# Kernel optimization log

Measured on AMD Instinct MI355X. Metric: run time of the kernel, lower is better.

## Reference

```python
import jax, jax.numpy as jnp
import numpy as np


def conv_transpose_4s2p1(x, w, b):
    # torch ConvTranspose2d(k=4, s=2, p=1). w is torch layout [Cin, Cout, 4, 4].
    # Equivalent to a regular conv with lhs_dilation=2, per-side pad k-1-p=2,
    # spatially-flipped kernel and in/out channels swapped.
    wk = jnp.flip(w, (2, 3)).transpose(1, 0, 2, 3)  # [Cout, Cin, 4, 4]
    y = jax.lax.conv_general_dilated(
        x, wk, window_strides=(1, 1), padding=((2, 2), (2, 2)),
        lhs_dilation=(2, 2), dimension_numbers=('NCHW', 'OIHW', 'NCHW'))
    return y + b[None, :, None, None]


def pac_conv_transpose_3s1p1(y, guide, w, b):
    # PacConvTranspose2d(k=3, s=1, p=1): with stride 1 this equals pacconv2d on
    # input zero-padded by k-1-p = 1, with the weight in/out-permuted and flipped
    # (pacnet native impl). Adaptive kernel: K_kk = exp(-0.5*||g_nbr - g_center||^2)
    # computed on the (zero-padded) guide at output resolution.
    B, C, H, W = y.shape
    wk = jnp.flip(w, (2, 3)).transpose(1, 0, 2, 3)  # [Cout, Cin, 3, 3]
    Co = wk.shape[0]
    gp = jnp.pad(guide, ((0, 0), (0, 0), (1, 1), (1, 1)))
    yp = jnp.pad(y, ((0, 0), (0, 0), (1, 1), (1, 1)))
    out = jnp.zeros((B, Co, H, W), y.dtype)
    for i in range(3):  # fixed 3x3 taps, not a data-dim loop
        for j in range(3):
            gn = gp[:, :, i:i + H, j:j + W]                # [B,Cg,H,W] neighbor
            d = gn - guide
            k = jnp.exp(-0.5 * jnp.sum(d * d, axis=1))      # [B,H,W] gaussian kernel
            yn = yp[:, :, i:i + H, j:j + W]                # [B,C,H,W]
            out = out + jnp.einsum('oc,bchw->bohw', wk[:, :, i, j], yn * k[:, None])
    return out + b[None, :, None, None]


def setup_inputs() -> dict:
    key = jax.random.key(0)
    k1, k2, k3, k4, k5, k6 = jax.random.split(key, 6)
    B, Cin, Cout, H, W = 4, 256, 128, 64, 64
    x = jax.random.normal(k1, (B, Cin, H, W), jnp.float32)
    # guide scaled so ||diff||^2 over 128 channels stays O(1-10) and the
    # gaussian kernel is not numerically degenerate
    guide = 0.08 * jax.random.normal(k2, (B, Cout, 2 * H, 2 * W), jnp.float32)
    w1 = jax.random.normal(k3, (Cin, Cout, 4, 4), jnp.float32) / np.sqrt(Cin * 16)
    b1 = 0.01 * jax.random.normal(k4, (Cout,), jnp.float32)
    w2 = jax.random.normal(k5, (Cout, Cout, 3, 3), jnp.float32) / np.sqrt(Cout * 9)
    b2 = 0.01 * jax.random.normal(k6, (Cout,), jnp.float32)
    return {'x': x, 'guide': guide, 'w1': w1, 'b1': b1, 'w2': w2, 'b2': b2}


def reference(x, guide, w1, b1, w2, b2):
    y = conv_transpose_4s2p1(x, w1, b1)          # [B, Cout, 2H, 2W]
    out = pac_conv_transpose_3s1p1(y, guide, w2, b2)
    return out
```

## Files before the change

### kernel.cpp

```cpp
#include <hip/hip_runtime.h>

#define B_  4
#define C1  256
#define C2  128
#define HH  64
#define WW  64
#define H2  128
#define W2  128

using short8  = __attribute__((ext_vector_type(8))) short;
using floatx4 = __attribute__((ext_vector_type(4))) float;
typedef unsigned short ushort_t;

#define W1C_OFF 0u
#define W1C_ELEMS (4 * 4 * 128 * 256)
#define W2C_OFF (W1C_ELEMS * 2u)
#define W2C_ELEMS (9 * 128 * 128)
#define KG_OFF  (W2C_OFF + W2C_ELEMS * 2u)
#define KG_ELEMS (B_ * H2 * 9 * W2)
#define XT_OFF  (KG_OFF + KG_ELEMS * 4u)
#define XT_ELEMS (B_ * HH * WW * C1)
#define Y_OFF   (XT_OFF + XT_ELEMS * 2u)
#define Y_ELEMS (B_ * H2 * W2 * C2)

static __device__ __forceinline__ ushort_t f2bf(float f) {
    union { float f; unsigned u; } v; v.f = f;
    unsigned r = v.u + 0x7FFFu + ((v.u >> 16) & 1u);
    return (ushort_t)(r >> 16);
}

__global__ void w1c_kernel(const float* __restrict__ w1, ushort_t* __restrict__ w1c) {
    int i = blockIdx.x * 256 + threadIdx.x;
    const int ci  = i & 255;
    const int co  = (i >> 8) & 127;
    const int tap = (i >> 15) & 3;
    const int cls = i >> 17;
    const int kh  = (cls >> 1) + 2 * (tap >> 1);
    const int kw  = (cls & 1) + 2 * (tap & 1);
    w1c[i] = f2bf(w1[((ci * C2 + co) * 4 + kh) * 4 + kw]);
}

__global__ void w2c_kernel(const float* __restrict__ w2, ushort_t* __restrict__ w2c) {
    int i = blockIdx.x * 256 + threadIdx.x;
    const int ci  = i & 127;
    const int o   = (i >> 7) & 127;
    const int tap = i >> 14;
    const int fi  = 2 - tap / 3;
    const int fj  = 2 - tap % 3;
    w2c[i] = f2bf(w2[((ci * C2 + o) * 3 + fi) * 3 + fj]);
}

__global__ __launch_bounds__(256) void xt_kernel(const float* __restrict__ x,
                                                 ushort_t* __restrict__ xT) {
    const int ih = blockIdx.x;
    const int b  = blockIdx.y;
    const int tid = threadIdx.x;
    __shared__ ushort_t tile[64 * 72];

    for (int chunk = 0; chunk < 4; ++chunk) {
        const int ci0 = chunk * 64;
        if (chunk) __syncthreads();
#pragma unroll
        for (int it = 0; it < 16; ++it) {
            const int cc = it * 4 + (tid >> 6);
            const int iw = tid & 63;
            const float v = x[(((size_t)b * C1 + ci0 + cc) * HH + ih) * WW + iw];
            tile[iw * 72 + cc] = f2bf(v);
        }
        __syncthreads();
#pragma unroll
        for (int it = 0; it < 2; ++it) {
            const int i  = it * 256 + tid;
            const int iw = i >> 3;
            const int t  = i & 7;
            const int4 v = *reinterpret_cast<const int4*>(&tile[iw * 72 + t * 8]);
            *reinterpret_cast<int4*>(&xT[(((size_t)(b * HH + ih) * WW) + iw) * C1 + ci0 + t * 8]) = v;
        }
    }
}

__global__ __launch_bounds__(512) void k_kernel(const float* __restrict__ guide,
                                                float* __restrict__ kg) {
    const int h = blockIdx.x;
    const int b = blockIdx.y;
    const int tid = threadIdx.x;
    const int cq  = tid >> 7;
    const int n   = tid & 127;

    float acc[9];
#pragma unroll
    for (int t = 0; t < 9; ++t) acc[t] = 0.f;

    const float* gb = guide + (size_t)b * C2 * H2 * W2;
    for (int c = cq * 32; c < cq * 32 + 32; ++c) {
        const float* grow = gb + (c * H2 + h) * W2;
        const float gc = grow[n];
#pragma unroll
        for (int di = 0; di < 3; ++di) {
            const int hh = h + di - 1;
            const bool rv = (hh >= 0) && (hh < H2);
            const float* gr = gb + (c * H2 + (rv ? hh : 0)) * W2;
#pragma unroll
            for (int dj = 0; dj < 3; ++dj) {
                const int col = n + dj - 1;
                const bool cv = rv && (col >= 0) && (col < W2);
                const float gn = cv ? gr[col] : 0.f;
                const float d = gn - gc;
                acc[di * 3 + dj] += d * d;
            }
        }
    }

    __shared__ float part[4][9][128];
#pragma unroll
    for (int t = 0; t < 9; ++t) part[cq][t][n] = acc[t];
    __syncthreads();

    for (int i = tid; i < 1152; i += 512) {
        const int t  = i >> 7;
        const int nn = i & 127;
        const float s = part[0][t][nn] + part[1][t][nn] + part[2][t][nn] + part[3][t][nn];
        kg[(size_t)(b * H2 + h) * 1152 + i] = __expf(-0.5f * s);
    }
}

__global__ __launch_bounds__(256, 2) void deconv_mfma(const ushort_t* __restrict__ xT,
                                                      const ushort_t* __restrict__ w1c,
                                                      const float* __restrict__ b1,
                                                      ushort_t* __restrict__ y) {
    const int pwc = blockIdx.x;
    const int pr  = blockIdx.y;
    const int b   = blockIdx.z;
    const int base_oh = (pr >> 1) * 4 + (pr & 1);
    const int p    = (base_oh + 1) & 1;
    const int ihA0 = (base_oh + 1 - p) >> 1;
    const int pwp  = 1 - pwc;
    const int cls  = p * 2 + pwp;

    const int tid  = threadIdx.x;
    const int lane = tid & 63;
    const int wave = tid >> 6;
    const int wm   = (wave & 1) * 64;
    const int wn   = (wave >> 1) * 64;
    const int quad = lane >> 4;
    const int l15  = lane & 15;

    __shared__ __align__(16) ushort_t lds[2 * 128 * 72];
    ushort_t* As = lds;
    ushort_t* Bs = lds + 128 * 72;

    floatx4 acc[4][4];
#pragma unroll
    for (int mi = 0; mi < 4; ++mi)
#pragma unroll
        for (int ni = 0; ni < 4; ++ni) acc[mi][ni] = (floatx4)0.f;

    for (int kc = 0; kc < 4; ++kc) {
        const int ci0 = kc * 64;
        for (int tap = 0; tap < 4; ++tap) {
            const int th = tap >> 1, tw = tap & 1;
            __syncthreads();
#pragma unroll
            for (int it = 0; it < 4; ++it) {
                const int i   = it * 256 + tid;
                const int row = i >> 3;
                const int t   = i & 7;
                const int4 v = *reinterpret_cast<const int4*>(
                    &w1c[((size_t)(cls * 4 + tap) * 128 + row) * 256 + ci0 + t * 8]);
                *reinterpret_cast<int4*>(&As[row * 72 + t * 8]) = v;
            }
#pragma unroll
            for (int it = 0; it < 4; ++it) {
                const int i   = it * 256 + tid;
                const int row = i >> 3;
                const int t   = i & 7;
                const int rh  = row >> 6;
                const int n64 = row & 63;
                const int ih  = ihA0 + rh - th;
                const int iw  = n64 + pwc - tw;
                int4 v = make_int4(0, 0, 0, 0);
                if (ih >= 0 && ih < HH && iw >= 0 && iw < WW)
                    v = *reinterpret_cast<const int4*>(
                        &xT[(((size_t)(b * HH + ih) * WW) + iw) * C1 + ci0 + t * 8]);
                *reinterpret_cast<int4*>(&Bs[row * 72 + t * 8]) = v;
            }
            __syncthreads();
#pragma unroll
            for (int k2 = 0; k2 < 2; ++k2) {
                short8 af[4], bfr[4];
#pragma unroll
                for (int mi = 0; mi < 4; ++mi)
                    af[mi] = *reinterpret_cast<const short8*>(
                        &As[(wm + mi * 16 + l15) * 72 + k2 * 32 + quad * 8]);
#pragma unroll
                for (int ni = 0; ni < 4; ++ni)
                    bfr[ni] = *reinterpret_cast<const short8*>(
                        &Bs[(wn + ni * 16 + l15) * 72 + k2 * 32 + quad * 8]);
#pragma unroll
                for (int mi = 0; mi < 4; ++mi)
#pragma unroll
                    for (int ni = 0; ni < 4; ++ni)
                        acc[mi][ni] = __builtin_amdgcn_mfma_f32_16x16x32_bf16(
                            af[mi], bfr[ni], acc[mi][ni], 0, 0, 0);
            }
        }
    }

    __syncthreads();
    ushort_t* Ot = lds;
#pragma unroll
    for (int mi = 0; mi < 4; ++mi)
#pragma unroll
        for (int ni = 0; ni < 4; ++ni) {
            const int n = wn + ni * 16 + l15;
#pragma unroll
            for (int r = 0; r < 4; ++r) {
                const int co = wm + mi * 16 + quad * 4 + r;
                Ot[n * 136 + co] = f2bf(acc[mi][ni][r] + b1[co]);
            }
        }
    __syncthreads();
#pragma unroll
    for (int it = 0; it < 8; ++it) {
        const int i   = it * 256 + tid;
        const int n   = i >> 4;
        const int t   = i & 15;
        const int rh  = n >> 6;
        const int n64 = n & 63;
        const int oh  = base_oh + 2 * rh;
        const int ow  = 2 * n64 + pwc;
        const int4 v = *reinterpret_cast<const int4*>(&Ot[n * 136 + t * 8]);
        *reinterpret_cast<int4*>(&y[(((size_t)(b * H2 + oh) * W2) + ow) * C2 + t * 8]) = v;
    }
}

__global__ __launch_bounds__(256, 2) void pac_mfma(const ushort_t* __restrict__ y,
                                                   const float* __restrict__ kg,
                                                   const ushort_t* __restrict__ w2c,
                                                   const float* __restrict__ b2,
                                                   float* __restrict__ out) {
    const int h = blockIdx.x;
    const int b = blockIdx.y;

    const int tid  = threadIdx.x;
    const int lane = tid & 63;
    const int wave = tid >> 6;
    const int wm   = (wave & 1) * 64;
    const int wn   = (wave >> 1) * 64;
    const int quad = lane >> 4;
    const int l15  = lane & 15;

    __shared__ __align__(16) ushort_t As[128 * 136];
    __shared__ __align__(16) ushort_t Ys[130 * 136];
    __shared__ float k_lds[9 * 128];

    for (int i = tid; i < 1152; i += 256)
        k_lds[i] = kg[(size_t)(b * H2 + h) * 1152 + i];

    float out_acc[4][4][4];
#pragma unroll
    for (int mi = 0; mi < 4; ++mi)
#pragma unroll
        for (int ni = 0; ni < 4; ++ni)
#pragma unroll
            for (int r = 0; r < 4; ++r) out_acc[mi][ni][r] = 0.f;

    for (int di = 0; di < 3; ++di) {
        const int hh = h + di - 1;
        if (hh < 0 || hh >= H2) continue;
        __syncthreads();
#pragma unroll
        for (int it = 0; it < 8; ++it) {
            const int i  = it * 256 + tid;
            const int r  = i >> 4;
            const int t  = i & 15;
            const int4 v = *reinterpret_cast<const int4*>(
                &y[(((size_t)(b * H2 + hh) * W2) + r) * C2 + t * 8]);
            *reinterpret_cast<int4*>(&Ys[(r + 1) * 136 + t * 8]) = v;
        }
        if (tid < 32) {
            const int ra = (tid < 16) ? 0 : 129;
            const int t  = tid & 15;
            *reinterpret_cast<int4*>(&Ys[ra * 136 + t * 8]) = make_int4(0, 0, 0, 0);
        }

        for (int dj = 0; dj < 3; ++dj) {
            const int tap = di * 3 + dj;
            __syncthreads();
#pragma unroll
            for (int it = 0; it < 8; ++it) {
                const int i   = it * 256 + tid;
                const int row = i >> 4;
                const int t   = i & 15;
                const int4 v = *reinterpret_cast<const int4*>(
                    &w2c[((size_t)tap * 128 + row) * 128 + t * 8]);
                *reinterpret_cast<int4*>(&As[row * 136 + t * 8]) = v;
            }
            __syncthreads();

            floatx4 acc[4][4];
#pragma unroll
            for (int mi = 0; mi < 4; ++mi)
#pragma unroll
                for (int ni = 0; ni < 4; ++ni) acc[mi][ni] = (floatx4)0.f;

#pragma unroll
            for (int kc = 0; kc < 4; ++kc) {
                short8 af[4], bfr[4];
#pragma unroll
                for (int mi = 0; mi < 4; ++mi)
                    af[mi] = *reinterpret_cast<const short8*>(
                        &As[(wm + mi * 16 + l15) * 136 + kc * 32 + quad * 8]);
#pragma unroll
                for (int ni = 0; ni < 4; ++ni)
                    bfr[ni] = *reinterpret_cast<const short8*>(
                        &Ys[(wn + ni * 16 + l15 + dj) * 136 + kc * 32 + quad * 8]);
#pragma unroll
                for (int mi = 0; mi < 4; ++mi)
#pragma unroll
                    for (int ni = 0; ni < 4; ++ni)
                        acc[mi][ni] = __builtin_amdgcn_mfma_f32_16x16x32_bf16(
                            af[mi], bfr[ni], acc[mi][ni], 0, 0, 0);
            }
            float kv[4];
#pragma unroll
            for (int ni = 0; ni < 4; ++ni)
                kv[ni] = k_lds[tap * 128 + wn + ni * 16 + l15];
#pragma unroll
            for (int mi = 0; mi < 4; ++mi)
#pragma unroll
                for (int ni = 0; ni < 4; ++ni)
#pragma unroll
                    for (int r = 0; r < 4; ++r)
                        out_acc[mi][ni][r] += kv[ni] * acc[mi][ni][r];
        }
    }

#pragma unroll
    for (int mi = 0; mi < 4; ++mi)
#pragma unroll
        for (int ni = 0; ni < 4; ++ni) {
            const int w = wn + ni * 16 + l15;
#pragma unroll
            for (int r = 0; r < 4; ++r) {
                const int o = wm + mi * 16 + quad * 4 + r;
                out[(((size_t)b * C2 + o) * H2 + h) * W2 + w] = out_acc[mi][ni][r] + b2[o];
            }
        }
}

extern "C" void kernel_launch(void* const* d_in, const int* in_sizes, int n_in,
                              void* d_out, int out_size, void* d_ws, size_t ws_size,
                              hipStream_t stream) {
    const float* x     = (const float*)d_in[0];
    const float* guide = (const float*)d_in[1];
    const float* w1    = (const float*)d_in[2];
    const float* b1    = (const float*)d_in[3];
    const float* w2    = (const float*)d_in[4];
    const float* b2    = (const float*)d_in[5];
    float* out = (float*)d_out;

    ushort_t* w1c = (ushort_t*)((char*)d_ws + W1C_OFF);
    ushort_t* w2c = (ushort_t*)((char*)d_ws + W2C_OFF);
    float*    kg  = (float*)((char*)d_ws + KG_OFF);
    ushort_t* xT  = (ushort_t*)((char*)d_ws + XT_OFF);
    ushort_t* y   = (ushort_t*)((char*)d_ws + Y_OFF);

    w1c_kernel<<<W1C_ELEMS / 256, 256, 0, stream>>>(w1, w1c);
    w2c_kernel<<<W2C_ELEMS / 256, 256, 0, stream>>>(w2, w2c);
    xt_kernel<<<dim3(HH, B_), 256, 0, stream>>>(x, xT);
    k_kernel<<<dim3(H2, B_), 512, 0, stream>>>(guide, kg);
    deconv_mfma<<<dim3(2, 64, B_), 256, 0, stream>>>(xT, w1c, b1, y);
    pac_mfma<<<dim3(H2, B_), 256, 0, stream>>>(y, kg, w2c, b2, out);
}
```

Measured before the change: 209.8 us.

## Read GEMM weight fragments directly from global memory and stage full-K activations

Both MFMA kernels now load the A (weight) fragments straight from global/L2 memory instead of staging them through LDS. The deconv kernel stages all 256 input channels of B per tap in one LDS buffer, and the PAC kernel drops its per-tap weight LDS copy, which removes most barriers. The weight-conversion kernels are rewritten for coalesced vector reads, and the transpose kernel now converts to bf16 after the LDS transpose. The trade is fewer syncs and less LDS traffic against higher global/L2 load latency on the MFMA operand path, which can now stall the matrix instructions.

New measurement: 227.7 us. 1.09x slower.

```diff
diff --git a/kernel.cpp b/kernel.cpp
--- a/kernel.cpp
+++ b/kernel.cpp
@@ -29,25 +29,39 @@
     return (ushort_t)(r >> 16);
 }
 
-__global__ void w1c_kernel(const float* __restrict__ w1, ushort_t* __restrict__ w1c) {
-    int i = blockIdx.x * 256 + threadIdx.x;
-    const int ci  = i & 255;
-    const int co  = (i >> 8) & 127;
-    const int tap = (i >> 15) & 3;
-    const int cls = i >> 17;
-    const int kh  = (cls >> 1) + 2 * (tap >> 1);
-    const int kw  = (cls & 1) + 2 * (tap & 1);
-    w1c[i] = f2bf(w1[((ci * C2 + co) * 4 + kh) * 4 + kw]);
-}
-
-__global__ void w2c_kernel(const float* __restrict__ w2, ushort_t* __restrict__ w2c) {
-    int i = blockIdx.x * 256 + threadIdx.x;
-    const int ci  = i & 127;
-    const int o   = (i >> 7) & 127;
-    const int tap = i >> 14;
-    const int fi  = 2 - tap / 3;
-    const int fj  = 2 - tap % 3;
-    w2c[i] = f2bf(w2[((ci * C2 + o) * 3 + fi) * 3 + fj]);
+__global__ __launch_bounds__(256) void w1c_kernel(const float* __restrict__ w1,
+                                                  ushort_t* __restrict__ w1c) {
+    const int co = blockIdx.x;
+    const int ci = threadIdx.x;
+    float v[16];
+#pragma unroll
+    for (int q = 0; q < 4; ++q) {
+        const float4 f = *reinterpret_cast<const float4*>(&w1[(ci * C2 + co) * 16 + q * 4]);
+        v[q * 4 + 0] = f.x; v[q * 4 + 1] = f.y; v[q * 4 + 2] = f.z; v[q * 4 + 3] = f.w;
+    }
+#pragma unroll
+    for (int cls = 0; cls < 4; ++cls)
+#pragma unroll
+        for (int tap = 0; tap < 4; ++tap) {
+            const int kh = (cls >> 1) + 2 * (tap >> 1);
+            const int kw = (cls & 1) + 2 * (tap & 1);
+            w1c[((cls * 4 + tap) * 128 + co) * 256 + ci] = f2bf(v[kh * 4 + kw]);
+        }
+}
+
+__global__ __launch_bounds__(256) void w2c_kernel(const float* __restrict__ w2,
+                                                  ushort_t* __restrict__ w2c) {
+    const int o  = blockIdx.x * 2 + (threadIdx.x >> 7);
+    const int ci = threadIdx.x & 127;
+    float v[9];
+#pragma unroll
+    for (int t = 0; t < 9; ++t) v[t] = w2[(ci * C2 + o) * 9 + t];
+#pragma unroll
+    for (int tap = 0; tap < 9; ++tap) {
+        const int fi = 2 - tap / 3;
+        const int fj = 2 - tap % 3;
+        w2c[((size_t)tap * 128 + o) * 128 + ci] = f2bf(v[fi * 3 + fj]);
+    }
 }
 
 __global__ __launch_bounds__(256) void xt_kernel(const float* __restrict__ x,
@@ -55,7 +69,7 @@
     const int ih = blockIdx.x;
     const int b  = blockIdx.y;
     const int tid = threadIdx.x;
-    __shared__ ushort_t tile[64 * 72];
+    __shared__ float tile[64 * 65];
 
     for (int chunk = 0; chunk < 4; ++chunk) {
         const int ci0 = chunk * 64;
@@ -64,8 +78,7 @@
         for (int it = 0; it < 16; ++it) {
             const int cc = it * 4 + (tid >> 6);
             const int iw = tid & 63;
-            const float v = x[(((size_t)b * C1 + ci0 + cc) * HH + ih) * WW + iw];
-            tile[iw * 72 + cc] = f2bf(v);
+            tile[iw * 65 + cc] = x[(((size_t)b * C1 + ci0 + cc) * HH + ih) * WW + iw];
         }
         __syncthreads();
 #pragma unroll
@@ -73,8 +86,11 @@
             const int i  = it * 256 + tid;
             const int iw = i >> 3;
             const int t  = i & 7;
-            const int4 v = *reinterpret_cast<const int4*>(&tile[iw * 72 + t * 8]);
-            *reinterpret_cast<int4*>(&xT[(((size_t)(b * HH + ih) * WW) + iw) * C1 + ci0 + t * 8]) = v;
+            ushort_t pk[8];
+#pragma unroll
+            for (int j = 0; j < 8; ++j) pk[j] = f2bf(tile[iw * 65 + t * 8 + j]);
+            *reinterpret_cast<int4*>(&xT[(((size_t)(b * HH + ih) * WW) + iw) * C1 + ci0 + t * 8]) =
+                *reinterpret_cast<const int4*>(pk);
         }
     }
 }
@@ -145,9 +161,7 @@
     const int quad = lane >> 4;
     const int l15  = lane & 15;
 
-    __shared__ __align__(16) ushort_t lds[2 * 128 * 72];
-    ushort_t* As = lds;
-    ushort_t* Bs = lds + 128 * 72;
+    __shared__ __align__(16) ushort_t lds[128 * 264];
 
     floatx4 acc[4][4];
 #pragma unroll
@@ -155,47 +169,41 @@
 #pragma unroll
         for (int ni = 0; ni < 4; ++ni) acc[mi][ni] = (floatx4)0.f;
 
-    for (int kc = 0; kc < 4; ++kc) {
-        const int ci0 = kc * 64;
-        for (int tap = 0; tap < 4; ++tap) {
-            const int th = tap >> 1, tw = tap & 1;
-            __syncthreads();
-#pragma unroll
-            for (int it = 0; it < 4; ++it) {
-                const int i   = it * 256 + tid;
-                const int row = i >> 3;
-                const int t   = i & 7;
-                const int4 v = *reinterpret_cast<const int4*>(
-                    &w1c[((size_t)(cls * 4 + tap) * 128 + row) * 256 + ci0 + t * 8]);
-                *reinterpret_cast<int4*>(&As[row * 72 + t * 8]) = v;
-            }
-#pragma unroll
-            for (int it = 0; it < 4; ++it) {
-                const int i   = it * 256 + tid;
-                const int row = i >> 3;
-                const int t   = i & 7;
-                const int rh  = row >> 6;
-                const int n64 = row & 63;
-                const int ih  = ihA0 + rh - th;
-                const int iw  = n64 + pwc - tw;
-                int4 v = make_int4(0, 0, 0, 0);
-                if (ih >= 0 && ih < HH && iw >= 0 && iw < WW)
-                    v = *reinterpret_cast<const int4*>(
-                        &xT[(((size_t)(b * HH + ih) * WW) + iw) * C1 + ci0 + t * 8]);
-                *reinterpret_cast<int4*>(&Bs[row * 72 + t * 8]) = v;
-            }
-            __syncthreads();
+    for (int tap = 0; tap < 4; ++tap) {
+        const int th = tap >> 1, tw = tap & 1;
+        __syncthreads();
+#pragma unroll
+        for (int it = 0; it < 16; ++it) {
+            const int i   = it * 256 + tid;
+            const int row = i >> 5;
+            const int t   = i & 31;
+            const int rh  = row >> 6;
+            const int n64 = row & 63;
+            const int ih  = ihA0 + rh - th;
+            const int iw  = n64 + pwc - tw;
+            int4 v = make_int4(0, 0, 0, 0);
+            if (ih >= 0 && ih < HH && iw >= 0 && iw < WW)
+                v = *reinterpret_cast<const int4*>(
+                    &xT[(((size_t)(b * HH + ih) * WW) + iw) * C1 + t * 8]);
+            *reinterpret_cast<int4*>(&lds[row * 264 + t * 8]) = v;
+        }
+        __syncthreads();
+
+        const ushort_t* wsrc = w1c + (size_t)(cls * 4 + tap) * 128 * 256;
+#pragma unroll
+        for (int kc = 0; kc < 4; ++kc) {
 #pragma unroll
             for (int k2 = 0; k2 < 2; ++k2) {
+                const int ko = kc * 64 + k2 * 32 + quad * 8;
                 short8 af[4], bfr[4];
 #pragma unroll
                 for (int mi = 0; mi < 4; ++mi)
                     af[mi] = *reinterpret_cast<const short8*>(
-                        &As[(wm + mi * 16 + l15) * 72 + k2 * 32 + quad * 8]);
+                        &wsrc[(wm + mi * 16 + l15) * 256 + ko]);
 #pragma unroll
                 for (int ni = 0; ni < 4; ++ni)
                     bfr[ni] = *reinterpret_cast<const short8*>(
-                        &Bs[(wn + ni * 16 + l15) * 72 + k2 * 32 + quad * 8]);
+                        &lds[(wn + ni * 16 + l15) * 264 + ko]);
 #pragma unroll
                 for (int mi = 0; mi < 4; ++mi)
 #pragma unroll
@@ -250,7 +258,6 @@
     const int quad = lane >> 4;
     const int l15  = lane & 15;
 
-    __shared__ __align__(16) ushort_t As[128 * 136];
     __shared__ __align__(16) ushort_t Ys[130 * 136];
     __shared__ float k_lds[9 * 128];
 
@@ -283,20 +290,11 @@
             const int t  = tid & 15;
             *reinterpret_cast<int4*>(&Ys[ra * 136 + t * 8]) = make_int4(0, 0, 0, 0);
         }
+        __syncthreads();
 
         for (int dj = 0; dj < 3; ++dj) {
             const int tap = di * 3 + dj;
-            __syncthreads();
-#pragma unroll
-            for (int it = 0; it < 8; ++it) {
-                const int i   = it * 256 + tid;
-                const int row = i >> 4;
-                const int t   = i & 15;
-                const int4 v = *reinterpret_cast<const int4*>(
-                    &w2c[((size_t)tap * 128 + row) * 128 + t * 8]);
-                *reinterpret_cast<int4*>(&As[row * 136 + t * 8]) = v;
-            }
-            __syncthreads();
+            const ushort_t* wsrc = w2c + (size_t)tap * 128 * 128;
 
             floatx4 acc[4][4];
 #pragma unroll
@@ -306,15 +304,16 @@
 
 #pragma unroll
             for (int kc = 0; kc < 4; ++kc) {
+                const int ko = kc * 32 + quad * 8;
                 short8 af[4], bfr[4];
 #pragma unroll
                 for (int mi = 0; mi < 4; ++mi)
                     af[mi] = *reinterpret_cast<const short8*>(
-                        &As[(wm + mi * 16 + l15) * 136 + kc * 32 + quad * 8]);
+                        &wsrc[(wm + mi * 16 + l15) * 128 + ko]);
 #pragma unroll
                 for (int ni = 0; ni < 4; ++ni)
                     bfr[ni] = *reinterpret_cast<const short8*>(
-                        &Ys[(wn + ni * 16 + l15 + dj) * 136 + kc * 32 + quad * 8]);
+                        &Ys[(wn + ni * 16 + l15 + dj) * 136 + ko]);
 #pragma unroll
                 for (int mi = 0; mi < 4; ++mi)
 #pragma unroll
@@ -366,8 +365,8 @@
     ushort_t* xT  = (ushort_t*)((char*)d_ws + XT_OFF);
     ushort_t* y   = (ushort_t*)((char*)d_ws + Y_OFF);
 
-    w1c_kernel<<<W1C_ELEMS / 256, 256, 0, stream>>>(w1, w1c);
-    w2c_kernel<<<W2C_ELEMS / 256, 256, 0, stream>>>(w2, w2c);
+    w1c_kernel<<<128, 256, 0, stream>>>(w1, w1c);
+    w2c_kernel<<<64, 256, 0, stream>>>(w2, w2c);
     xt_kernel<<<dim3(HH, B_), 256, 0, stream>>>(x, xT);
     k_kernel<<<dim3(H2, B_), 512, 0, stream>>>(guide, kg);
     deconv_mfma<<<dim3(2, 64, B_), 256, 0, stream>>>(xT, w1c, b1, y);
```
